# Kernel tuning notes

Hardware: AMD Instinct MI355X
Metric: run time of the kernel (lower is better)

The kernel has to match this reference:

```python
import jax, jax.numpy as jnp
import numpy as np

N_HEADS = 2
WINDOW = 4
BLOCK = 256


def _get_rel_emb(emb, length):
    # emb: [1, 2*WINDOW+1, K] -> [1, 2*length-1, K]
    pad = max(length - (WINDOW + 1), 0)
    start = max((WINDOW + 1) - length, 0)
    e = jnp.pad(emb, ((0, 0), (pad, pad), (0, 0)))
    return e[:, start:start + 2 * length - 1]


def _rel_to_abs(x):
    # x: [b, h, l, 2l-1] -> [b, h, l, l] (skew trick)
    b, h, l, _ = x.shape
    x = jnp.pad(x, ((0, 0), (0, 0), (0, 0), (0, 1))).reshape(b, h, 2 * l * l)
    x = jnp.pad(x, ((0, 0), (0, 0), (0, l - 1))).reshape(b, h, l + 1, 2 * l - 1)
    return x[:, :, :l, l - 1:]


def _abs_to_rel(x):
    # x: [b, h, l, l] -> [b, h, l, 2l-1] (inverse skew)
    b, h, l, _ = x.shape
    x = jnp.pad(x, ((0, 0), (0, 0), (0, 0), (0, l - 1))).reshape(b, h, l * (2 * l - 1))
    x = jnp.pad(x, ((0, 0), (0, 0), (l, 0))).reshape(b, h, l, 2 * l)
    return x[:, :, :, 1:]


def _attention(x, c, attn_mask, Wq, bq, Wk, bk, Wv, bv, Wo, bo, emb_rel_k, emb_rel_v):
    B, C, T = x.shape
    H, K = N_HEADS, C // N_HEADS
    # projections (torch Linear on [B,T,C])
    q = (jnp.einsum('bct,cd->btd', x, Wq) + bq).reshape(B, T, H, K).transpose(0, 2, 1, 3)
    k = (jnp.einsum('bct,cd->btd', c, Wk) + bk).reshape(B, T, H, K).transpose(0, 2, 1, 3)
    v = (jnp.einsum('bct,cd->btd', c, Wv) + bv).reshape(B, T, H, K).transpose(0, 2, 1, 3)
    qs = q / jnp.sqrt(jnp.float32(K))
    scores = jnp.einsum('bhtk,bhsk->bhts', qs, k)  # [B,H,T,T]
    # relative-position key logits (heads_share=True -> single table)
    rel_k = _get_rel_emb(emb_rel_k, T)[0]          # [2T-1, K]
    rel_logits = jnp.einsum('bhtk,rk->bhtr', qs, rel_k)
    scores = scores + _rel_to_abs(rel_logits)
    # proximal bias: -log1p(|i-j|)
    r = jnp.arange(T, dtype=jnp.float32)
    scores = scores - jnp.log1p(jnp.abs(r[:, None] - r[None, :]))[None, None]
    # attn mask + block-local mask (block mask active because mask is given)
    ij = jnp.arange(T)
    block_ok = jnp.abs(ij[:, None] - ij[None, :]) <= BLOCK
    valid = (attn_mask != 0) & block_ok[None, None]
    scores = jnp.where(valid, scores, jnp.float32(-1e4))
    p = jax.nn.softmax(scores, axis=-1)
    out = jnp.einsum('bhts,bhsk->bhtk', p, v)
    # relative-position value contribution
    rel_v = _get_rel_emb(emb_rel_v, T)[0]          # [2T-1, K]
    out = out + jnp.einsum('bhtr,rk->bhtk', _abs_to_rel(p), rel_v)
    out = out.transpose(0, 2, 1, 3).reshape(B, T, C)
    y = jnp.einsum('btd,do->bto', out, Wo) + bo
    return y.transpose(0, 2, 1)  # [B, out_channels, T]


def setup_inputs() -> dict:
    key = jax.random.key(0)
    ks = jax.random.split(key, 8)
    B, C, T = 4, 192, 2048
    K = C // N_HEADS
    s = jnp.float32(0.05)
    rel_std = jnp.float32(K ** -0.5)
    return {
        'x': jax.random.normal(ks[0], (B, C, T), jnp.float32),
        'c': jax.random.normal(ks[1], (B, C, T), jnp.float32),
        'Wq': jax.random.normal(ks[2], (C, C), jnp.float32) * s,
        'bq': jnp.zeros((C,), jnp.float32),
        'Wk': jax.random.normal(ks[3], (C, C), jnp.float32) * s,
        'bk': jnp.zeros((C,), jnp.float32),
        'Wv': jax.random.normal(ks[4], (C, C), jnp.float32) * s,
        'bv': jnp.zeros((C,), jnp.float32),
        'Wo': jax.random.normal(ks[5], (C, C), jnp.float32) * s,
        'bo': jnp.zeros((C,), jnp.float32),
        'emb_rel_k': jax.random.normal(ks[6], (1, 2 * WINDOW + 1, K), jnp.float32) * rel_std,
        'emb_rel_v': jax.random.normal(ks[7], (1, 2 * WINDOW + 1, K), jnp.float32) * rel_std,
        'attn_mask': jnp.ones((B, 1, T, T), jnp.int32),
    }


def reference(x, c, Wq, bq, Wk, bk, Wv, bv, Wo, bo, emb_rel_k, emb_rel_v, attn_mask):
    return _attention(x, c, attn_mask, Wq, bq, Wk, bk, Wv, bv, Wo, bo, emb_rel_k, emb_rel_v)
```

## Files before the change

### kernel.cpp

```cpp
#include <hip/hip_runtime.h>
#include <hip/hip_bf16.h>

#define B_DIM 4
#define C_DIM 192
#define T_SEQ 2048
#define H_DIM 2
#define K_DIM 96
#define BAND 256
#define IT 16
#define WSLOT 544
#define W_P 548
#define PMW 17

typedef __attribute__((ext_vector_type(8))) short bf16x8;
typedef __attribute__((ext_vector_type(4))) short bf16x4;
typedef __attribute__((ext_vector_type(4))) float f32x4;
#define MFMA16 __builtin_amdgcn_mfma_f32_16x16x32_bf16

__device__ __forceinline__ float bfbits2f(short s) {
    union { short s; __hip_bfloat16 h; } u; u.s = s; return __bfloat162float(u.h);
}
__device__ __forceinline__ short f2bf_bits(float f) {
    union { __hip_bfloat16 h; short s; } u; u.h = __float2bfloat16(f); return u.s;
}

#define OFF_WT(m)  ((size_t)(m)*73728)
#define OFF_BQS    ((size_t)294912)
#define OFF_RELKBF ((size_t)295680)
#define OFF_PM     ((size_t)298752)
#define OFF_QBF    ((size_t)855808)
#define OFF_KBF    (OFF_QBF + 3145728)
#define OFF_VTB    (OFF_KBF + 3145728)
#define OFF_OBTC   (OFF_VTB + 3145728)

__global__ __launch_bounds__(256)
void prep_kernel(const float* __restrict__ Wq, const float* __restrict__ Wk,
                 const float* __restrict__ Wv, const float* __restrict__ Wo,
                 const float* __restrict__ bq, const float* __restrict__ relk,
                 const int* __restrict__ mask, char* __restrict__ ws)
{
    const float qscale = 0.10206207261596577f;
    const int bidx = blockIdx.x;
    const int tid  = threadIdx.x;

    if (bidx < 576) {
        const size_t idx = (size_t)bidx*256 + tid;
        const int mi  = (int)(idx / 36864);
        const int rem = (int)(idx % 36864);
        const int c = rem / C_DIM, d = rem % C_DIM;
        const float* src = (mi == 0) ? Wq : (mi == 1) ? Wk : (mi == 2) ? Wv : Wo;
        float v = src[c*C_DIM + d];
        if (mi == 0) v *= qscale;
        ((short*)(ws + OFF_WT(mi)))[d*C_DIM + c] = f2bf_bits(v);
        return;
    }
    if (bidx < 1120) {
        const int idx = (bidx - 576)*256 + tid;
        const int b = idx / (T_SEQ*PMW);
        const int rem = idx % (T_SEQ*PMW);
        const int i = rem / PMW, w = rem % PMW;
        const int jlo = max(0, (i & ~15) - BAND);
        const int* mrow = mask + ((size_t)b*T_SEQ + i)*T_SEQ;
        unsigned bits = 0;
        #pragma unroll
        for (int g4 = 0; g4 < 8; ++g4) {
            const int jg = jlo + 32*w + 4*g4;
            if (jg + 3 < T_SEQ) {
                const int4 mv = *reinterpret_cast<const int4*>(mrow + jg);
                bits |= (unsigned)(mv.x != 0) << (4*g4);
                bits |= (unsigned)(mv.y != 0) << (4*g4+1);
                bits |= (unsigned)(mv.z != 0) << (4*g4+2);
                bits |= (unsigned)(mv.w != 0) << (4*g4+3);
            } else {
                #pragma unroll
                for (int e = 0; e < 4; ++e)
                    if (jg + e < T_SEQ && mrow[jg+e] != 0) bits |= 1u << (4*g4+e);
            }
        }
        ((unsigned*)(ws + OFF_PM))[idx] = bits;
        return;
    }
    if (tid < C_DIM)
        ((float*)(ws + OFF_BQS))[tid] = bq[tid]*qscale;
    short* rkb = (short*)(ws + OFF_RELKBF);
    for (int idx = tid; idx < 16*K_DIM; idx += 256) {
        const int row = idx / K_DIM;
        rkb[idx] = (row < 9) ? f2bf_bits(relk[idx]) : (short)0;
    }
}

__global__ __launch_bounds__(256)
void proj_kernel(const float* __restrict__ x, const float* __restrict__ cin,
                 const float* __restrict__ bk, const float* __restrict__ bv,
                 char* __restrict__ ws)
{
    __shared__ short xs[IT*C_DIM];
    __shared__ short cs[IT*C_DIM];
    const int b   = blockIdx.x >> 7;
    const int t0  = (blockIdx.x & 127) * IT;
    const int tid = threadIdx.x;
    const int wave = tid >> 6, lane = tid & 63;
    const int q4 = lane >> 4, lr = lane & 15;

    for (int l = tid; l < 768; l += 256) {
        const int cr = l >> 2, u = l & 3;
        const size_t off = (size_t)(b*C_DIM + cr)*T_SEQ + t0 + 4*u;
        const float4 xv = *reinterpret_cast<const float4*>(x + off);
        const float4 cv = *reinterpret_cast<const float4*>(cin + off);
        xs[(4*u+0)*C_DIM + cr] = f2bf_bits(xv.x);
        xs[(4*u+1)*C_DIM + cr] = f2bf_bits(xv.y);
        xs[(4*u+2)*C_DIM + cr] = f2bf_bits(xv.z);
        xs[(4*u+3)*C_DIM + cr] = f2bf_bits(xv.w);
        cs[(4*u+0)*C_DIM + cr] = f2bf_bits(cv.x);
        cs[(4*u+1)*C_DIM + cr] = f2bf_bits(cv.y);
        cs[(4*u+2)*C_DIM + cr] = f2bf_bits(cv.z);
        cs[(4*u+3)*C_DIM + cr] = f2bf_bits(cv.w);
    }
    __syncthreads();

    const short* WqT = (const short*)(ws + OFF_WT(0));
    const short* WkT = (const short*)(ws + OFF_WT(1));
    const short* WvT = (const short*)(ws + OFF_WT(2));

    f32x4 qa[3], ka[3], va[3];
    #pragma unroll
    for (int j = 0; j < 3; ++j) {
        qa[j] = (f32x4){0,0,0,0}; ka[j] = (f32x4){0,0,0,0}; va[j] = (f32x4){0,0,0,0};
    }
    for (int kc = 0; kc < 6; ++kc) {
        const int ko = kc*32 + q4*8;
        const bf16x8 xf = *reinterpret_cast<const bf16x8*>(xs + lr*C_DIM + ko);
        const bf16x8 cf = *reinterpret_cast<const bf16x8*>(cs + lr*C_DIM + ko);
        #pragma unroll
        for (int j = 0; j < 3; ++j) {
            const int dt = 3*wave + j;
            const bf16x8 wqf = *reinterpret_cast<const bf16x8*>(WqT + (dt*16 + lr)*C_DIM + ko);
            const bf16x8 wkf = *reinterpret_cast<const bf16x8*>(WkT + (dt*16 + lr)*C_DIM + ko);
            const bf16x8 wvf = *reinterpret_cast<const bf16x8*>(WvT + (dt*16 + lr)*C_DIM + ko);
            qa[j] = MFMA16(xf, wqf, qa[j], 0, 0, 0);
            ka[j] = MFMA16(cf, wkf, ka[j], 0, 0, 0);
            va[j] = MFMA16(wvf, cf, va[j], 0, 0, 0);
        }
    }

    const float* bqs = (const float*)(ws + OFF_BQS);
    short* qbf = (short*)(ws + OFF_QBF);
    short* kbf = (short*)(ws + OFF_KBF);
    short* vtb = (short*)(ws + OFF_VTB);
    #pragma unroll
    for (int j = 0; j < 3; ++j) {
        const int dt = 3*wave + j;
        {
            const int d = dt*16 + lr, h = d/K_DIM, kk = d%K_DIM;
            const int bh = b*H_DIM + h;
            const float bq_v = bqs[d], bk_v = bk[d];
            #pragma unroll
            for (int e = 0; e < 4; ++e) {
                const int t = t0 + q4*4 + e;
                const size_t off = ((size_t)bh*T_SEQ + t)*K_DIM + kk;
                qbf[off] = f2bf_bits(qa[j][e] + bq_v);
                kbf[off] = f2bf_bits(ka[j][e] + bk_v);
            }
        }
        {
            #pragma unroll
            for (int e = 0; e < 4; ++e) {
                const int d = dt*16 + q4*4 + e, h = d/K_DIM, kk = d%K_DIM;
                const int bh = b*H_DIM + h;
                vtb[((size_t)bh*K_DIM + kk)*T_SEQ + t0 + lr] = f2bf_bits(va[j][e] + bv[d]);
            }
        }
    }
}

__global__ __launch_bounds__(256)
void attn_kernel(const float* __restrict__ relv, char* __restrict__ ws)
{
    __shared__ float p_s[IT*W_P];
    __shared__ float shbuf[864];

    const short* qbf = (const short*)(ws + OFF_QBF);
    const short* kbf = (const short*)(ws + OFF_KBF);
    const short* vtb = (const short*)(ws + OFF_VTB);
    const short* rkb = (const short*)(ws + OFF_RELKBF);
    const unsigned* pm = (const unsigned*)(ws + OFF_PM);
    short* obtc = (short*)(ws + OFF_OBTC);

    const int bh  = blockIdx.x >> 7;
    const int i0  = (blockIdx.x & 127) * IT;
    const int b   = bh / H_DIM;
    const int h   = bh % H_DIM;
    const int tid = threadIdx.x;
    const int wave = tid >> 6, lane = tid & 63;
    const int q4 = lane >> 4, lr = lane & 15;

    const int jlo  = max(0, i0 - BAND);
    const int jhi  = min(T_SEQ - 1, i0 + IT - 1 + BAND);
    const int wlen = jhi - jlo + 1;
    const size_t qkv_base = (size_t)bh * T_SEQ * K_DIM;

    float* lt = shbuf;
    float* rl = shbuf + 260;
    for (int idx = tid; idx < 257; idx += 256) lt[idx] = log1pf((float)idx);

    bf16x8 qa[3];
    {
        const short* qrow = qbf + qkv_base + (size_t)(i0 + lr)*K_DIM + q4*8;
        #pragma unroll
        for (int kc = 0; kc < 3; ++kc)
            qa[kc] = *reinterpret_cast<const bf16x8*>(qrow + kc*32);
    }

    for (int jt = wave; jt < WSLOT/16; jt += 4) {
        int jr = jlo + jt*16 + lr;
        if (jr > T_SEQ-1) jr = T_SEQ-1;
        const short* krow = kbf + qkv_base + (size_t)jr*K_DIM + q4*8;
        f32x4 s = {0.f,0.f,0.f,0.f};
        #pragma unroll
        for (int kc = 0; kc < 3; ++kc)
            s = MFMA16(qa[kc], *reinterpret_cast<const bf16x8*>(krow + kc*32), s, 0, 0, 0);
        #pragma unroll
        for (int e = 0; e < 4; ++e)
            p_s[(q4*4 + e)*W_P + jt*16 + lr] = s[e];
    }
    if (wave == 3) {
        const short* krow = rkb + lr*K_DIM + q4*8;
        f32x4 s = {0.f,0.f,0.f,0.f};
        #pragma unroll
        for (int kc = 0; kc < 3; ++kc)
            s = MFMA16(qa[kc], *reinterpret_cast<const bf16x8*>(krow + kc*32), s, 0, 0, 0);
        if (lr < 9) {
            #pragma unroll
            for (int e = 0; e < 4; ++e)
                rl[(q4*4 + e)*9 + lr] = s[e];
        }
    }
    __syncthreads();

    {
        const int r = tid >> 4, sj = tid & 15;
        const int i = i0 + r;
        const int pmrow = (b*T_SEQ + i)*PMW;
        float vals[36];
        float m = -INFINITY;
        #pragma unroll
        for (int mm = 0; mm < 9; ++mm) {
            const int j0 = 4*sj + 64*mm;
            float4 pv = make_float4(0.f,0.f,0.f,0.f);
            unsigned mb = 0;
            if (j0 < WSLOT) {
                pv = *reinterpret_cast<const float4*>(p_s + r*W_P + j0);
                mb = pm[pmrow + (j0 >> 5)] >> (j0 & 31);
            }
            const float pe[4] = {pv.x, pv.y, pv.z, pv.w};
            #pragma unroll
            for (int e = 0; e < 4; ++e) {
                const int j = j0 + e;
                float val = -INFINITY;
                if (j0 < WSLOT && j < wlen) {
                    const int jg = jlo + j, dd = jg - i;
                    const int ad = dd < 0 ? -dd : dd;
                    if (ad <= BAND && ((mb >> e) & 1)) {
                        val = pe[e] - lt[ad];
                        if ((unsigned)(dd + 4) <= 8u) val += rl[r*9 + dd + 4];
                    }
                }
                vals[mm*4 + e] = val;
                m = fmaxf(m, val);
            }
        }
        #pragma unroll
        for (int off = 8; off > 0; off >>= 1) m = fmaxf(m, __shfl_xor(m, off, 64));
        if (m == -INFINITY) m = 0.f;
        float ssum = 0.f;
        #pragma unroll
        for (int u = 0; u < 36; ++u) { vals[u] = __expf(vals[u] - m); ssum += vals[u]; }
        #pragma unroll
        for (int off = 8; off > 0; off >>= 1) ssum += __shfl_xor(ssum, off, 64);
        const float inv = ssum > 0.f ? 1.f/ssum : 0.f;
        short* pb = (short*)p_s;
        #pragma unroll
        for (int mm = 0; mm < 9; ++mm) {
            const int j0 = 4*sj + 64*mm;
            if (j0 < WSLOT) {
                bf16x4 w;
                #pragma unroll
                for (int e = 0; e < 4; ++e) w[e] = f2bf_bits(vals[mm*4+e]*inv);
                *reinterpret_cast<bf16x4*>(pb + r*(2*W_P) + j0) = w;
            }
        }
    }
    __syncthreads();

    for (int idx = tid; idx < 9*K_DIM; idx += 256) shbuf[idx] = relv[idx];

    const short* pb = (const short*)p_s;
    f32x4 o0 = {0.f,0.f,0.f,0.f}, o1 = {0.f,0.f,0.f,0.f};
    for (int kc = 0; kc < WSLOT/32; ++kc) {
        const bf16x8 pa = *reinterpret_cast<const bf16x8*>(pb + lr*(2*W_P) + kc*32 + q4*8);
        int tc = jlo + kc*32 + q4*8;
        if (tc > T_SEQ-8) tc = T_SEQ-8;
        const bf16x8 vb0 = *reinterpret_cast<const bf16x8*>(
            vtb + qkv_base + (size_t)(wave*16 + lr)*T_SEQ + tc);
        o0 = MFMA16(pa, vb0, o0, 0, 0, 0);
        if (wave < 2) {
            const bf16x8 vb1 = *reinterpret_cast<const bf16x8*>(
                vtb + qkv_base + (size_t)((wave+4)*16 + lr)*T_SEQ + tc);
            o1 = MFMA16(pa, vb1, o1, 0, 0, 0);
        }
    }
    __syncthreads();

    #pragma unroll
    for (int u = 0; u < 2; ++u) {
        if (u == 1 && wave >= 2) break;
        const int nt = (u == 0) ? wave : wave + 4;
        const f32x4 oc = (u == 0) ? o0 : o1;
        const int col = nt*16 + lr;
        #pragma unroll
        for (int e = 0; e < 4; ++e) {
            const int row = q4*4 + e;
            const int i = i0 + row;
            float v = oc[e];
            #pragma unroll
            for (int dd = 0; dd < 9; ++dd) {
                const int jg = i + dd - 4;
                if (jg >= 0 && jg < T_SEQ)
                    v += bfbits2f(pb[row*(2*W_P) + (jg - jlo)]) * shbuf[dd*K_DIM + col];
            }
            obtc[((size_t)b*T_SEQ + i)*C_DIM + h*K_DIM + col] = f2bf_bits(v);
        }
    }
}

__global__ __launch_bounds__(256)
void oproj_kernel(const float* __restrict__ bo, float* __restrict__ y,
                  const char* __restrict__ ws)
{
    const int b   = blockIdx.x >> 7;
    const int t0  = (blockIdx.x & 127) * 16;
    const int tid = threadIdx.x;
    const int wave = tid >> 6, lane = tid & 63;
    const int q4 = lane >> 4, lr = lane & 15;

    const short* WoT  = (const short*)(ws + OFF_WT(3));
    const short* obtc = (const short*)(ws + OFF_OBTC);

    f32x4 a[3];
    #pragma unroll
    for (int j = 0; j < 3; ++j) a[j] = (f32x4){0.f,0.f,0.f,0.f};
    for (int kc = 0; kc < 6; ++kc) {
        const int ko = kc*32 + q4*8;
        const bf16x8 bf = *reinterpret_cast<const bf16x8*>(
            obtc + ((size_t)b*T_SEQ + t0 + lr)*C_DIM + ko);
        #pragma unroll
        for (int j = 0; j < 3; ++j) {
            const bf16x8 af = *reinterpret_cast<const bf16x8*>(
                WoT + ((3*wave + j)*16 + lr)*C_DIM + ko);
            a[j] = MFMA16(af, bf, a[j], 0, 0, 0);
        }
    }
    #pragma unroll
    for (int j = 0; j < 3; ++j) {
        #pragma unroll
        for (int e = 0; e < 4; ++e) {
            const int d = (3*wave + j)*16 + q4*4 + e;
            y[((size_t)b*C_DIM + d)*T_SEQ + t0 + lr] = a[j][e] + bo[d];
        }
    }
}

extern "C" void kernel_launch(void* const* d_in, const int* in_sizes, int n_in,
                              void* d_out, int out_size, void* d_ws, size_t ws_size,
                              hipStream_t stream)
{
    const float* x    = (const float*)d_in[0];
    const float* c    = (const float*)d_in[1];
    const float* Wq   = (const float*)d_in[2];
    const float* bq   = (const float*)d_in[3];
    const float* Wk   = (const float*)d_in[4];
    const float* bk   = (const float*)d_in[5];
    const float* Wv   = (const float*)d_in[6];
    const float* bv   = (const float*)d_in[7];
    const float* Wo   = (const float*)d_in[8];
    const float* bo   = (const float*)d_in[9];
    const float* relk = (const float*)d_in[10];
    const float* relv = (const float*)d_in[11];
    const int*   mask = (const int*)d_in[12];
    float*       y    = (float*)d_out;
    char*        ws   = (char*)d_ws;

    hipLaunchKernelGGL(prep_kernel, dim3(1121), dim3(256), 0, stream,
                       Wq, Wk, Wv, Wo, bq, relk, mask, ws);
    hipLaunchKernelGGL(proj_kernel, dim3(B_DIM*(T_SEQ/16)), dim3(256), 0, stream,
                       x, c, bk, bv, ws);
    hipLaunchKernelGGL(attn_kernel, dim3(B_DIM*H_DIM*(T_SEQ/IT)), dim3(256), 0, stream,
                       relv, ws);
    hipLaunchKernelGGL(oproj_kernel, dim3(B_DIM*(T_SEQ/16)), dim3(256), 0, stream,
                       bo, y, ws);
}
```

Before: 179.8 us.

## Split projection grids, prefetch K/V fragments, stage mask in LDS, precompute log table

The projection and output-projection kernels now launch twice as many blocks, each handling half the output channels, to raise occupancy. The attention kernel software-prefetches the next K and V fragments before issuing MFMAs. It copies the per-row mask bits into shared memory once instead of reading them from global memory in the softmax loop. The log1p table is now computed once in the prep kernel and loaded from the workspace. In exchange, the projection kernel re-stages x/c into LDS twice, and the prefetch adds register pressure.

```diff
diff --git a/kernel.cpp b/kernel.cpp
--- a/kernel.cpp
+++ b/kernel.cpp
@@ -27,8 +27,9 @@
 #define OFF_WT(m)  ((size_t)(m)*73728)
 #define OFF_BQS    ((size_t)294912)
 #define OFF_RELKBF ((size_t)295680)
-#define OFF_PM     ((size_t)298752)
-#define OFF_QBF    ((size_t)855808)
+#define OFF_LT     ((size_t)298752)
+#define OFF_PM     ((size_t)299840)
+#define OFF_QBF    ((size_t)856896)
 #define OFF_KBF    (OFF_QBF + 3145728)
 #define OFF_VTB    (OFF_KBF + 3145728)
 #define OFF_OBTC   (OFF_VTB + 3145728)
@@ -87,6 +88,8 @@
         const int row = idx / K_DIM;
         rkb[idx] = (row < 9) ? f2bf_bits(relk[idx]) : (short)0;
     }
+    float* ltws = (float*)(ws + OFF_LT);
+    for (int idx = tid; idx < 257; idx += 256) ltws[idx] = log1pf((float)idx);
 }
 
 __global__ __launch_bounds__(256)
@@ -96,9 +99,10 @@
 {
     __shared__ short xs[IT*C_DIM];
     __shared__ short cs[IT*C_DIM];
-    const int b   = blockIdx.x >> 7;
-    const int t0  = (blockIdx.x & 127) * IT;
-    const int tid = threadIdx.x;
+    const int b    = blockIdx.x >> 8;
+    const int half = (blockIdx.x >> 7) & 1;
+    const int t0   = (blockIdx.x & 127) * IT;
+    const int tid  = threadIdx.x;
     const int wave = tid >> 6, lane = tid & 63;
     const int q4 = lane >> 4, lr = lane & 15;
 
@@ -121,35 +125,29 @@
     const short* WqT = (const short*)(ws + OFF_WT(0));
     const short* WkT = (const short*)(ws + OFF_WT(1));
     const short* WvT = (const short*)(ws + OFF_WT(2));
-
-    f32x4 qa[3], ka[3], va[3];
-    #pragma unroll
-    for (int j = 0; j < 3; ++j) {
-        qa[j] = (f32x4){0,0,0,0}; ka[j] = (f32x4){0,0,0,0}; va[j] = (f32x4){0,0,0,0};
-    }
-    for (int kc = 0; kc < 6; ++kc) {
-        const int ko = kc*32 + q4*8;
-        const bf16x8 xf = *reinterpret_cast<const bf16x8*>(xs + lr*C_DIM + ko);
-        const bf16x8 cf = *reinterpret_cast<const bf16x8*>(cs + lr*C_DIM + ko);
-        #pragma unroll
-        for (int j = 0; j < 3; ++j) {
-            const int dt = 3*wave + j;
-            const bf16x8 wqf = *reinterpret_cast<const bf16x8*>(WqT + (dt*16 + lr)*C_DIM + ko);
-            const bf16x8 wkf = *reinterpret_cast<const bf16x8*>(WkT + (dt*16 + lr)*C_DIM + ko);
-            const bf16x8 wvf = *reinterpret_cast<const bf16x8*>(WvT + (dt*16 + lr)*C_DIM + ko);
-            qa[j] = MFMA16(xf, wqf, qa[j], 0, 0, 0);
-            ka[j] = MFMA16(cf, wkf, ka[j], 0, 0, 0);
-            va[j] = MFMA16(wvf, cf, va[j], 0, 0, 0);
-        }
-    }
-
     const float* bqs = (const float*)(ws + OFF_BQS);
     short* qbf = (short*)(ws + OFF_QBF);
     short* kbf = (short*)(ws + OFF_KBF);
     short* vtb = (short*)(ws + OFF_VTB);
+
     #pragma unroll
-    for (int j = 0; j < 3; ++j) {
-        const int dt = 3*wave + j;
+    for (int u = 0; u < 2; ++u) {
+        if (u == 1 && wave >= 2) break;
+        const int tl = (u == 0) ? wave : wave + 4;
+        const int dt = half*6 + tl;
+        f32x4 qa = {0,0,0,0}, ka = {0,0,0,0}, va = {0,0,0,0};
+        #pragma unroll
+        for (int kc = 0; kc < 6; ++kc) {
+            const int ko = kc*32 + q4*8;
+            const bf16x8 xf = *reinterpret_cast<const bf16x8*>(xs + lr*C_DIM + ko);
+            const bf16x8 cf = *reinterpret_cast<const bf16x8*>(cs + lr*C_DIM + ko);
+            const bf16x8 wqf = *reinterpret_cast<const bf16x8*>(WqT + (dt*16 + lr)*C_DIM + ko);
+            const bf16x8 wkf = *reinterpret_cast<const bf16x8*>(WkT + (dt*16 + lr)*C_DIM + ko);
+            const bf16x8 wvf = *reinterpret_cast<const bf16x8*>(WvT + (dt*16 + lr)*C_DIM + ko);
+            qa = MFMA16(xf, wqf, qa, 0, 0, 0);
+            ka = MFMA16(cf, wkf, ka, 0, 0, 0);
+            va = MFMA16(wvf, cf, va, 0, 0, 0);
+        }
         {
             const int d = dt*16 + lr, h = d/K_DIM, kk = d%K_DIM;
             const int bh = b*H_DIM + h;
@@ -158,8 +156,8 @@
             for (int e = 0; e < 4; ++e) {
                 const int t = t0 + q4*4 + e;
                 const size_t off = ((size_t)bh*T_SEQ + t)*K_DIM + kk;
-                qbf[off] = f2bf_bits(qa[j][e] + bq_v);
-                kbf[off] = f2bf_bits(ka[j][e] + bk_v);
+                qbf[off] = f2bf_bits(qa[e] + bq_v);
+                kbf[off] = f2bf_bits(ka[e] + bk_v);
             }
         }
         {
@@ -167,7 +165,7 @@
             for (int e = 0; e < 4; ++e) {
                 const int d = dt*16 + q4*4 + e, h = d/K_DIM, kk = d%K_DIM;
                 const int bh = b*H_DIM + h;
-                vtb[((size_t)bh*K_DIM + kk)*T_SEQ + t0 + lr] = f2bf_bits(va[j][e] + bv[d]);
+                vtb[((size_t)bh*K_DIM + kk)*T_SEQ + t0 + lr] = f2bf_bits(va[e] + bv[d]);
             }
         }
     }
@@ -178,11 +176,13 @@
 {
     __shared__ float p_s[IT*W_P];
     __shared__ float shbuf[864];
+    __shared__ unsigned pml[IT*PMW];
 
     const short* qbf = (const short*)(ws + OFF_QBF);
     const short* kbf = (const short*)(ws + OFF_KBF);
     const short* vtb = (const short*)(ws + OFF_VTB);
     const short* rkb = (const short*)(ws + OFF_RELKBF);
+    const float* ltws = (const float*)(ws + OFF_LT);
     const unsigned* pm = (const unsigned*)(ws + OFF_PM);
     short* obtc = (short*)(ws + OFF_OBTC);
 
@@ -201,7 +201,9 @@
 
     float* lt = shbuf;
     float* rl = shbuf + 260;
-    for (int idx = tid; idx < 257; idx += 256) lt[idx] = log1pf((float)idx);
+    for (int idx = tid; idx < 257; idx += 256) lt[idx] = ltws[idx];
+    for (int idx = tid; idx < IT*PMW; idx += 256)
+        pml[idx] = pm[(b*T_SEQ + i0)*PMW + idx];
 
     bf16x8 qa[3];
     {
@@ -211,17 +213,38 @@
             qa[kc] = *reinterpret_cast<const bf16x8*>(qrow + kc*32);
     }
 
-    for (int jt = wave; jt < WSLOT/16; jt += 4) {
-        int jr = jlo + jt*16 + lr;
-        if (jr > T_SEQ-1) jr = T_SEQ-1;
-        const short* krow = kbf + qkv_base + (size_t)jr*K_DIM + q4*8;
-        f32x4 s = {0.f,0.f,0.f,0.f};
-        #pragma unroll
-        for (int kc = 0; kc < 3; ++kc)
-            s = MFMA16(qa[kc], *reinterpret_cast<const bf16x8*>(krow + kc*32), s, 0, 0, 0);
-        #pragma unroll
-        for (int e = 0; e < 4; ++e)
-            p_s[(q4*4 + e)*W_P + jt*16 + lr] = s[e];
+    {
+        int jt = wave;
+        const short* kr0;
+        {
+            int jr = jlo + jt*16 + lr;
+            if (jr > T_SEQ-1) jr = T_SEQ-1;
+            kr0 = kbf + qkv_base + (size_t)jr*K_DIM + q4*8;
+        }
+        bf16x8 kb0 = *reinterpret_cast<const bf16x8*>(kr0);
+        bf16x8 kb1 = *reinterpret_cast<const bf16x8*>(kr0 + 32);
+        bf16x8 kb2 = *reinterpret_cast<const bf16x8*>(kr0 + 64);
+        while (jt < WSLOT/16) {
+            const int jtn = jt + 4;
+            bf16x8 n0, n1, n2;
+            if (jtn < WSLOT/16) {
+                int jr = jlo + jtn*16 + lr;
+                if (jr > T_SEQ-1) jr = T_SEQ-1;
+                const short* krn = kbf + qkv_base + (size_t)jr*K_DIM + q4*8;
+                n0 = *reinterpret_cast<const bf16x8*>(krn);
+                n1 = *reinterpret_cast<const bf16x8*>(krn + 32);
+                n2 = *reinterpret_cast<const bf16x8*>(krn + 64);
+            }
+            f32x4 s = {0.f,0.f,0.f,0.f};
+            s = MFMA16(qa[0], kb0, s, 0, 0, 0);
+            s = MFMA16(qa[1], kb1, s, 0, 0, 0);
+            s = MFMA16(qa[2], kb2, s, 0, 0, 0);
+            #pragma unroll
+            for (int e = 0; e < 4; ++e)
+                p_s[(q4*4 + e)*W_P + jt*16 + lr] = s[e];
+            kb0 = n0; kb1 = n1; kb2 = n2;
+            jt = jtn;
+        }
     }
     if (wave == 3) {
         const short* krow = rkb + lr*K_DIM + q4*8;
@@ -240,7 +263,6 @@
     {
         const int r = tid >> 4, sj = tid & 15;
         const int i = i0 + r;
-        const int pmrow = (b*T_SEQ + i)*PMW;
         float vals[36];
         float m = -INFINITY;
         #pragma unroll
@@ -250,7 +272,7 @@
             unsigned mb = 0;
             if (j0 < WSLOT) {
                 pv = *reinterpret_cast<const float4*>(p_s + r*W_P + j0);
-                mb = pm[pmrow + (j0 >> 5)] >> (j0 & 31);
+                mb = pml[r*PMW + (j0 >> 5)] >> (j0 & 31);
             }
             const float pe[4] = {pv.x, pv.y, pv.z, pv.w};
             #pragma unroll
@@ -296,17 +318,27 @@
 
     const short* pb = (const short*)p_s;
     f32x4 o0 = {0.f,0.f,0.f,0.f}, o1 = {0.f,0.f,0.f,0.f};
-    for (int kc = 0; kc < WSLOT/32; ++kc) {
-        const bf16x8 pa = *reinterpret_cast<const bf16x8*>(pb + lr*(2*W_P) + kc*32 + q4*8);
-        int tc = jlo + kc*32 + q4*8;
-        if (tc > T_SEQ-8) tc = T_SEQ-8;
-        const bf16x8 vb0 = *reinterpret_cast<const bf16x8*>(
-            vtb + qkv_base + (size_t)(wave*16 + lr)*T_SEQ + tc);
-        o0 = MFMA16(pa, vb0, o0, 0, 0, 0);
-        if (wave < 2) {
-            const bf16x8 vb1 = *reinterpret_cast<const bf16x8*>(
-                vtb + qkv_base + (size_t)((wave+4)*16 + lr)*T_SEQ + tc);
-            o1 = MFMA16(pa, vb1, o1, 0, 0, 0);
+    {
+        auto vaddr = [&](int kcv)->const short* {
+            int tc = jlo + kcv*32 + q4*8;
+            if (tc > T_SEQ-8) tc = T_SEQ-8;
+            return vtb + qkv_base + (size_t)lr*T_SEQ + tc;
+        };
+        const short* va0 = vaddr(0);
+        bf16x8 vb0 = *reinterpret_cast<const bf16x8*>(va0 + (size_t)(wave*16)*T_SEQ);
+        bf16x8 vb1;
+        if (wave < 2) vb1 = *reinterpret_cast<const bf16x8*>(va0 + (size_t)((wave+4)*16)*T_SEQ);
+        for (int kc = 0; kc < WSLOT/32; ++kc) {
+            bf16x8 n0, n1;
+            if (kc + 1 < WSLOT/32) {
+                const short* van = vaddr(kc + 1);
+                n0 = *reinterpret_cast<const bf16x8*>(van + (size_t)(wave*16)*T_SEQ);
+                if (wave < 2) n1 = *reinterpret_cast<const bf16x8*>(van + (size_t)((wave+4)*16)*T_SEQ);
+            }
+            const bf16x8 pa = *reinterpret_cast<const bf16x8*>(pb + lr*(2*W_P) + kc*32 + q4*8);
+            o0 = MFMA16(pa, vb0, o0, 0, 0, 0);
+            if (wave < 2) o1 = MFMA16(pa, vb1, o1, 0, 0, 0);
+            vb0 = n0; vb1 = n1;
         }
     }
     __syncthreads();
@@ -337,35 +369,35 @@
 void oproj_kernel(const float* __restrict__ bo, float* __restrict__ y,
                   const char* __restrict__ ws)
 {
-    const int b   = blockIdx.x >> 7;
-    const int t0  = (blockIdx.x & 127) * 16;
-    const int tid = threadIdx.x;
+    const int b    = blockIdx.x >> 8;
+    const int half = (blockIdx.x >> 7) & 1;
+    const int t0   = (blockIdx.x & 127) * 16;
+    const int tid  = threadIdx.x;
     const int wave = tid >> 6, lane = tid & 63;
     const int q4 = lane >> 4, lr = lane & 15;
 
     const short* WoT  = (const short*)(ws + OFF_WT(3));
     const short* obtc = (const short*)(ws + OFF_OBTC);
 
-    f32x4 a[3];
     #pragma unroll
-    for (int j = 0; j < 3; ++j) a[j] = (f32x4){0.f,0.f,0.f,0.f};
-    for (int kc = 0; kc < 6; ++kc) {
-        const int ko = kc*32 + q4*8;
-        const bf16x8 bf = *reinterpret_cast<const bf16x8*>(
-            obtc + ((size_t)b*T_SEQ + t0 + lr)*C_DIM + ko);
-        #pragma unroll
-        for (int j = 0; j < 3; ++j) {
+    for (int u = 0; u < 2; ++u) {
+        if (u == 1 && wave >= 2) break;
+        const int tl = (u == 0) ? wave : wave + 4;
+        const int dt = half*6 + tl;
+        f32x4 a = {0.f,0.f,0.f,0.f};
+        #pragma unroll
+        for (int kc = 0; kc < 6; ++kc) {
+            const int ko = kc*32 + q4*8;
+            const bf16x8 bf = *reinterpret_cast<const bf16x8*>(
+                obtc + ((size_t)b*T_SEQ + t0 + lr)*C_DIM + ko);
             const bf16x8 af = *reinterpret_cast<const bf16x8*>(
-                WoT + ((3*wave + j)*16 + lr)*C_DIM + ko);
-            a[j] = MFMA16(af, bf, a[j], 0, 0, 0);
-        }
-    }
-    #pragma unroll
-    for (int j = 0; j < 3; ++j) {
+                WoT + (dt*16 + lr)*C_DIM + ko);
+            a = MFMA16(af, bf, a, 0, 0, 0);
+        }
         #pragma unroll
         for (int e = 0; e < 4; ++e) {
-            const int d = (3*wave + j)*16 + q4*4 + e;
-            y[((size_t)b*C_DIM + d)*T_SEQ + t0 + lr] = a[j][e] + bo[d];
+            const int d = dt*16 + q4*4 + e;
+            y[((size_t)b*C_DIM + d)*T_SEQ + t0 + lr] = a[e] + bo[d];
         }
     }
 }
@@ -392,10 +424,10 @@
 
     hipLaunchKernelGGL(prep_kernel, dim3(1121), dim3(256), 0, stream,
                        Wq, Wk, Wv, Wo, bq, relk, mask, ws);
-    hipLaunchKernelGGL(proj_kernel, dim3(B_DIM*(T_SEQ/16)), dim3(256), 0, stream,
+    hipLaunchKernelGGL(proj_kernel, dim3(B_DIM*2*(T_SEQ/16)), dim3(256), 0, stream,
                        x, c, bk, bv, ws);
     hipLaunchKernelGGL(attn_kernel, dim3(B_DIM*H_DIM*(T_SEQ/IT)), dim3(256), 0, stream,
                        relv, ws);
-    hipLaunchKernelGGL(oproj_kernel, dim3(B_DIM*(T_SEQ/16)), dim3(256), 0, stream,
+    hipLaunchKernelGGL(oproj_kernel, dim3(B_DIM*2*(T_SEQ/16)), dim3(256), 0, stream,
                        bo, y, ws);
 }
```

New measurement: 181.6 us. No clear change (+1.0%).
